# Optimization experiments

Measured on AMD Instinct MI355X. Metric: run time of the kernel, lower is better.

## Reference

```python
import jax, jax.numpy as jnp
import numpy as np

TOP_K = 2


def setup_inputs() -> dict:
    key = jax.random.key(0)
    ks = jax.random.split(key, 5)
    B, S, H, E, F = 4, 1024, 1024, 16, 4096
    scale = 0.02
    return {
        "input_tensor": jax.random.normal(ks[0], (B, S, H), dtype=jnp.float32),
        "Wg": scale * jax.random.normal(ks[1], (H, E), dtype=jnp.float32),
        "bg": jnp.zeros((E,), dtype=jnp.float32),
        "W1": scale * jax.random.normal(ks[2], (E, H, F), dtype=jnp.float32),
        "b1": jnp.zeros((E, F), dtype=jnp.float32),
        "W2": scale * jax.random.normal(ks[3], (E, F, H), dtype=jnp.float32),
        "b2": jnp.zeros((E, H), dtype=jnp.float32),
    }


def reference(input_tensor, Wg, bg, W1, b1, W2, b2):
    # Faithful to DualOutputMoE.forward_first_pass: the per-(b,s,k) Python loop
    # plus _weighted_sum collapses ALL token expert outputs into a single
    # [1,1,H] vector normalized by the total routing weight (= B*S).
    B, S, H = input_tensor.shape
    T = B * S
    E = Wg.shape[1]
    x = input_tensor.reshape(T, H)

    routing_scores = x @ Wg + bg                    # [T, E] (raw gate logits)
    top_v, top_i = jax.lax.top_k(routing_scores, TOP_K)
    top_w = jax.nn.softmax(top_v, axis=-1)          # per-token top-k weights

    # combine[t, e] = sum_k top_w[t, k] * 1[top_i[t, k] == e]
    combine = jnp.zeros((T, E), x.dtype).at[jnp.arange(T)[:, None], top_i].add(top_w)
    total_weight = top_w.sum()                      # matches python sum of .item()s

    def expert_step(acc, params):
        w1, bb1, w2, bb2, c = params                # c: [T] combine weights for this expert
        y = jax.nn.gelu(x @ w1 + bb1, approximate=False) @ w2 + bb2  # [T, H]
        return acc + c @ y, None

    acc0 = jnp.zeros((H,), x.dtype)
    acc, _ = jax.lax.scan(expert_step, acc0, (W1, b1, W2, b2, combine.T))
    first_output = (acc / total_weight).reshape(1, 1, H)
    return first_output
```

## Files before the change

kernel.cpp:

```cpp
#include <hip/hip_runtime.h>
#include <hip/hip_bf16.h>
#include <math.h>

typedef __bf16 bf16_t;
typedef __bf16 bf16x4 __attribute__((ext_vector_type(4)));
typedef __bf16 bf16x8 __attribute__((ext_vector_type(8)));
typedef float  f32x4  __attribute__((ext_vector_type(4)));

#define T_TOK 4096
#define H_DIM 1024
#define E_NUM 16
#define F_DIM 4096
#define CH_ROWS 128
#define CH_MAX  32

#define WS_E0     0
#define WS_E1     16384
#define WS_W0     32768
#define WS_W1     49152
#define WS_COUNTS 65536
#define WS_SUMW   65664
#define WS_XOFF   65792
#define WS_LIDX   131072
#define WS_LW     393216
#define WS_GPART  655360
#define WS_P2     655360
#define WS_G      9043968
#define WS_XE     9306112
#define WS_W1T    30277632
#define W1T_PER_E 8388608

#define AS_GLOBAL(p) ((const __attribute__((address_space(1))) void*)(p))
#define AS_LDS(p)    ((__attribute__((address_space(3))) void*)(p))

__global__ __launch_bounds__(64) void k_route(const float* __restrict__ x,
    const float* __restrict__ Wg, const float* __restrict__ bg,
    int* __restrict__ e0, int* __restrict__ e1,
    float* __restrict__ w0, float* __restrict__ w1)
{
    const int t = blockIdx.x;
    const int lane = threadIdx.x;
    const float* xr = x + (size_t)t * H_DIM;

    float s[E_NUM];
#pragma unroll
    for (int e = 0; e < E_NUM; ++e) s[e] = 0.f;

#pragma unroll
    for (int i = 0; i < 16; ++i) {
        const int h = i * 64 + lane;
        const float xv = xr[h];
        const float4* wr = (const float4*)(Wg + (size_t)h * E_NUM);
        float4 q0 = wr[0], q1 = wr[1], q2 = wr[2], q3 = wr[3];
        s[0] += xv*q0.x;  s[1] += xv*q0.y;  s[2] += xv*q0.z;  s[3] += xv*q0.w;
        s[4] += xv*q1.x;  s[5] += xv*q1.y;  s[6] += xv*q1.z;  s[7] += xv*q1.w;
        s[8] += xv*q2.x;  s[9] += xv*q2.y;  s[10]+= xv*q2.z;  s[11]+= xv*q2.w;
        s[12]+= xv*q3.x;  s[13]+= xv*q3.y;  s[14]+= xv*q3.z;  s[15]+= xv*q3.w;
    }
#pragma unroll
    for (int off = 32; off >= 1; off >>= 1) {
#pragma unroll
        for (int e = 0; e < E_NUM; ++e) s[e] += __shfl_xor(s[e], off);
    }
    if (lane == 0) {
#pragma unroll
        for (int e = 0; e < E_NUM; ++e) s[e] += bg[e];
        float b1v = -3e38f; int i1 = 0;
#pragma unroll
        for (int e = 0; e < E_NUM; ++e) { if (s[e] > b1v) { b1v = s[e]; i1 = e; } }
        float b2v = -3e38f; int i2 = 0;
#pragma unroll
        for (int e = 0; e < E_NUM; ++e) { if (e != i1 && s[e] > b2v) { b2v = s[e]; i2 = e; } }
        const float ex  = expf(b2v - b1v);
        const float inv = 1.f / (1.f + ex);
        e0[t] = i1; e1[t] = i2;
        w0[t] = inv; w1[t] = ex * inv;
    }
}

__global__ __launch_bounds__(64) void k_lists(const int* __restrict__ e0, const int* __restrict__ e1,
    const float* __restrict__ w0, const float* __restrict__ w1,
    int* __restrict__ lidx, float* __restrict__ lw,
    int* __restrict__ counts, float* __restrict__ sumw)
{
    const int e = blockIdx.x;
    const int lane = threadIdx.x;
    int cnt = 0; float sw = 0.f;
    for (int base = 0; base < T_TOK; base += 64) {
        const int t = base + lane;
        const bool m0 = (e0[t] == e);
        const bool m1 = (e1[t] == e);
        const bool m  = m0 | m1;
        const unsigned long long bal = __ballot(m);
        const int pos = cnt + __popcll(bal & ((1ull << lane) - 1ull));
        if (m) {
            const float w = m0 ? w0[t] : w1[t];
            lidx[e * T_TOK + pos] = t;
            lw[e * T_TOK + pos]   = w;
            sw += w;
        }
        cnt += __popcll(bal);
    }
#pragma unroll
    for (int off = 32; off >= 1; off >>= 1) sw += __shfl_xor(sw, off);
    if (lane == 0) { counts[e] = cnt; sumw[e] = sw; }
}

__global__ void k_scan(const int* __restrict__ counts, int* __restrict__ xoff) {
    if (threadIdx.x == 0) {
        int o = 0;
        for (int e = 0; e < E_NUM; ++e) { xoff[e] = o; o += (counts[e] + CH_ROWS - 1) & ~(CH_ROWS - 1); }
    }
}

__global__ __launch_bounds__(256) void k_gather(const float* __restrict__ x,
    const int* __restrict__ lidx, const int* __restrict__ counts,
    const int* __restrict__ xoff, bf16_t* __restrict__ Xe)
{
    const int chunk = blockIdx.x >> 1;
    const int part  = blockIdx.x & 1;
    const int e = blockIdx.y;
    const int cnt = counts[e];
    const int start = chunk * CH_ROWS;
    if (chunk && start >= cnt) return;
    const int tid = threadIdx.x;
    const size_t base = ((size_t)(xoff[e] >> 7) + chunk) * 131072;

    for (int it = 0; it < 32; ++it) {
        const int u    = part * 8192 + it * 256 + tid;
        const int kt   = u >> 10;
        const int wi   = u & 1023;
        const int rl   = wi >> 3;
        const int c    = wi & 7;
        const int row  = start + rl;
        bf16x8 v8 = {};
        if (row < cnt) {
            const int tok = lidx[e * T_TOK + row];
            const int cp  = c ^ (rl & 7);
            const int k   = kt * 64 + cp * 8;
            const float4 a = *(const float4*)(x + (size_t)tok * H_DIM + k);
            const float4 b = *(const float4*)(x + (size_t)tok * H_DIM + k + 4);
            v8[0]=(bf16_t)a.x; v8[1]=(bf16_t)a.y; v8[2]=(bf16_t)a.z; v8[3]=(bf16_t)a.w;
            v8[4]=(bf16_t)b.x; v8[5]=(bf16_t)b.y; v8[6]=(bf16_t)b.z; v8[7]=(bf16_t)b.w;
        }
        *(bf16x8*)(Xe + base + (size_t)kt * 8192 + rl * 64 + c * 8) = v8;
    }
}

__global__ __launch_bounds__(512, 1) void k_w1t(const float* __restrict__ W1,
    bf16_t* __restrict__ W1T, int ebase)
{
    const int kt = blockIdx.x;
    const int fq = blockIdx.y;
    const int ge = blockIdx.z;
    const int e  = ebase + ge;
    const int tid = threadIdx.x;

    __shared__ bf16_t S[64][1024];

    const float* src = W1 + (size_t)e * H_DIM * F_DIM + (size_t)(kt * 64) * F_DIM + fq * 1024;
    for (int it = 0; it < 32; ++it) {
        const int u   = it * 512 + tid;
        const int row = u >> 8;
        const int c4  = u & 255;
        const float4 v = *(const float4*)(src + (size_t)row * F_DIM + c4 * 4);
        bf16x4 b4; b4[0]=(bf16_t)v.x; b4[1]=(bf16_t)v.y; b4[2]=(bf16_t)v.z; b4[3]=(bf16_t)v.w;
        *(bf16x4*)&S[row][c4 * 4] = b4;
    }
    __syncthreads();

#pragma unroll
    for (int ot = 0; ot < 2; ++ot) {
        const int orow = ot * 512 + tid;
        const int ftl  = orow >> 7;
        const int f    = orow & 127;
        const int fg   = ftl * 128 + f;
        bf16_t kv[64];
#pragma unroll
        for (int k = 0; k < 64; ++k) kv[k] = S[k][fg];
        bf16_t* dst = W1T + ((((size_t)ge * 32 + (fq * 8 + ftl)) * 16 + kt) * 8192) + f * 64;
#pragma unroll
        for (int j = 0; j < 8; ++j) {
            bf16x8 pk;
#pragma unroll
            for (int q = 0; q < 8; ++q) pk[q] = kv[j * 8 + q];
            *(bf16x8*)&dst[((j ^ (f & 7)) * 8)] = pk;
        }
    }
}

__global__ __launch_bounds__(256, 2) void k_expert(
    const bf16_t* __restrict__ W1T, const float* __restrict__ b1,
    const bf16_t* __restrict__ Xe, const float* __restrict__ lw,
    const int* __restrict__ counts, const int* __restrict__ xoff,
    float* __restrict__ gpart, int ebase)
{
    const int ftile = blockIdx.x;
    const int chunk = blockIdx.y;
    const int ge    = blockIdx.z;
    const int e     = ebase + ge;
    const int cnt   = counts[e];
    const int start = chunk * CH_ROWS;
    if (chunk && start >= cnt) return;

    __shared__ __align__(16) bf16_t Alds[2][8192];
    __shared__ __align__(16) bf16_t Blds[2][8192];
    __shared__ float w_s[CH_ROWS];
    __shared__ float b1_s[128];
    __shared__ float gred[2][128];

    const int tid  = threadIdx.x;
    const int lane = tid & 63;
    const int wid  = tid >> 6;
    const int wm   = wid & 1;
    const int wn   = wid >> 1;
    const int lr   = lane & 15;
    const int lg   = lane >> 4;

    if (tid < CH_ROWS) {
        const int r = start + tid;
        w_s[tid] = (r < cnt) ? lw[e * T_TOK + r] : 0.f;
    }
    if (tid < 128) b1_s[tid] = b1[(size_t)e * F_DIM + ftile * 128 + tid];

    f32x4 acc[4][4];
#pragma unroll
    for (int i = 0; i < 4; ++i)
#pragma unroll
        for (int j = 0; j < 4; ++j)
#pragma unroll
            for (int q = 0; q < 4; ++q) acc[i][j][q] = 0.f;

    const bf16_t* XeSlab = Xe + ((size_t)(xoff[e] >> 7) + chunk) * 131072;
    const bf16_t* W1Slab = W1T + (((size_t)ge * 32 + ftile) * 16) * 8192;

#define STAGE(T, BUF) { \
    const bf16_t* sa = XeSlab + (size_t)(T) * 8192; \
    const bf16_t* sb = W1Slab + (size_t)(T) * 8192; \
    _Pragma("unroll") \
    for (int p = 0; p < 4; ++p) { \
        const int off = p * 2048 + wid * 512; \
        __builtin_amdgcn_global_load_lds(AS_GLOBAL(sa + off + lane * 8), AS_LDS(&Alds[BUF][off]), 16, 0, 0); \
        __builtin_amdgcn_global_load_lds(AS_GLOBAL(sb + off + lane * 8), AS_LDS(&Blds[BUF][off]), 16, 0, 0); \
    } }

#define COMPUTE(BUF) { \
    _Pragma("unroll") \
    for (int kh = 0; kh < 2; ++kh) { \
        bf16x8 af[4], bfr[4]; \
        _Pragma("unroll") \
        for (int mf = 0; mf < 4; ++mf) { \
            const int r = wm * 64 + mf * 16 + lr; \
            af[mf] = *(const bf16x8*)&Alds[BUF][r * 64 + (((kh << 2) | lg) ^ (r & 7)) * 8]; \
        } \
        _Pragma("unroll") \
        for (int nf = 0; nf < 4; ++nf) { \
            const int f = wn * 64 + nf * 16 + lr; \
            bfr[nf] = *(const bf16x8*)&Blds[BUF][f * 64 + (((kh << 2) | lg) ^ (f & 7)) * 8]; \
        } \
        _Pragma("unroll") \
        for (int mf = 0; mf < 4; ++mf) \
            _Pragma("unroll") \
            for (int nf = 0; nf < 4; ++nf) \
                acc[mf][nf] = __builtin_amdgcn_mfma_f32_16x16x32_bf16(af[mf], bfr[nf], acc[mf][nf], 0, 0, 0); \
    } }

    STAGE(0, 0);
    __syncthreads();

    int cur = 0;
#pragma unroll 2
    for (int t = 0; t < 16; ++t) {
        if (t < 15) { STAGE(t + 1, cur ^ 1); }
        __builtin_amdgcn_sched_barrier(0);
        COMPUTE(cur);
        __syncthreads();
        cur ^= 1;
    }
#undef STAGE
#undef COMPUTE

    float gcol[4] = {0.f, 0.f, 0.f, 0.f};
#pragma unroll
    for (int nf = 0; nf < 4; ++nf) {
        const float bb = b1_s[wn * 64 + nf * 16 + lr];
#pragma unroll
        for (int mf = 0; mf < 4; ++mf) {
#pragma unroll
            for (int i = 0; i < 4; ++i) {
                const int row = wm * 64 + mf * 16 + lg * 4 + i;
                const float h  = acc[mf][nf][i] + bb;
                const float gl = 0.5f * h * (1.f + erff(h * 0.70710678118654752f));
                gcol[nf] += w_s[row] * gl;
            }
        }
    }
#pragma unroll
    for (int nf = 0; nf < 4; ++nf) {
        gcol[nf] += __shfl_xor(gcol[nf], 16);
        gcol[nf] += __shfl_xor(gcol[nf], 32);
    }
    if (lane < 16) {
#pragma unroll
        for (int nf = 0; nf < 4; ++nf) gred[wm][wn * 64 + nf * 16 + lane] = gcol[nf];
    }
    __syncthreads();
    if (tid < 128) {
        const float sum = gred[0][tid] + gred[1][tid];
        gpart[(size_t)(e * CH_MAX + chunk) * F_DIM + ftile * 128 + tid] = sum;
    }
}

__global__ __launch_bounds__(256) void k_redg(const float* __restrict__ gpart,
    const int* __restrict__ counts, float* __restrict__ g)
{
    const int e = blockIdx.y;
    const int f = blockIdx.x * 256 + threadIdx.x;
    const int nch = (counts[e] + CH_ROWS - 1) / CH_ROWS;
    float s = 0.f;
    for (int c = 0; c < nch; ++c)
        s += gpart[(size_t)(e * CH_MAX + c) * F_DIM + f];
    g[(size_t)e * F_DIM + f] = s;
}

__global__ __launch_bounds__(256) void k_out1(const float* __restrict__ g,
    const float* __restrict__ W2, float* __restrict__ p2)
{
    const int fc = blockIdx.x;
    const int e  = blockIdx.y;
    const int tid = threadIdx.x;
    __shared__ float gs[128];
    if (tid < 128) gs[tid] = g[(size_t)e * F_DIM + fc * 128 + tid];
    __syncthreads();
    const float* W2p = W2 + (size_t)e * F_DIM * H_DIM + (size_t)fc * 128 * H_DIM;
    float ax = 0.f, ay = 0.f, az = 0.f, aw = 0.f;
#pragma unroll 8
    for (int f = 0; f < 128; ++f) {
        const float gv = gs[f];
        const float4 wv = *(const float4*)(W2p + (size_t)f * H_DIM + tid * 4);
        ax += gv * wv.x; ay += gv * wv.y; az += gv * wv.z; aw += gv * wv.w;
    }
    float4 st; st.x = ax; st.y = ay; st.z = az; st.w = aw;
    *(float4*)(p2 + (size_t)(e * 32 + fc) * H_DIM + tid * 4) = st;
}

__global__ __launch_bounds__(256) void k_out2(const float* __restrict__ p2,
    const float* __restrict__ sumw, const float* __restrict__ b2, float* __restrict__ out)
{
    const int tid = threadIdx.x;
    const int hh  = tid & 31;
    const int seg = tid >> 5;
    const int h   = blockIdx.x * 32 + hh;
    float s = 0.f;
    for (int j = 0; j < 64; ++j)
        s += p2[(size_t)(seg * 64 + j) * H_DIM + h];
    __shared__ float red[8][33];
    red[seg][hh] = s;
    __syncthreads();
    if (tid < 32) {
        const int h2 = blockIdx.x * 32 + tid;
        float tot = 0.f;
#pragma unroll
        for (int q = 0; q < 8; ++q) tot += red[q][tid];
        float tw = 0.f, bias = 0.f;
#pragma unroll
        for (int e = 0; e < E_NUM; ++e) { tw += sumw[e]; bias += sumw[e] * b2[e * H_DIM + h2]; }
        out[h2] = (tot + bias) / tw;
    }
}

extern "C" void kernel_launch(void* const* d_in, const int* in_sizes, int n_in,
                              void* d_out, int out_size, void* d_ws, size_t ws_size,
                              hipStream_t stream) {
    const float* x  = (const float*)d_in[0];
    const float* Wg = (const float*)d_in[1];
    const float* bg = (const float*)d_in[2];
    const float* W1 = (const float*)d_in[3];
    const float* b1 = (const float*)d_in[4];
    const float* W2 = (const float*)d_in[5];
    const float* b2 = (const float*)d_in[6];
    float* out = (float*)d_out;

    char* ws = (char*)d_ws;
    int*    e0     = (int*)(ws + WS_E0);
    int*    e1     = (int*)(ws + WS_E1);
    float*  w0     = (float*)(ws + WS_W0);
    float*  w1     = (float*)(ws + WS_W1);
    int*    counts = (int*)(ws + WS_COUNTS);
    float*  sumw   = (float*)(ws + WS_SUMW);
    int*    xoff   = (int*)(ws + WS_XOFF);
    int*    lidx   = (int*)(ws + WS_LIDX);
    float*  lw     = (float*)(ws + WS_LW);
    float*  gpart  = (float*)(ws + WS_GPART);
    float*  g      = (float*)(ws + WS_G);
    float*  p2     = (float*)(ws + WS_P2);
    bf16_t* Xe     = (bf16_t*)(ws + WS_XE);
    bf16_t* W1T    = (bf16_t*)(ws + WS_W1T);

    int cap = 1;
    if (ws_size > (size_t)WS_W1T + (size_t)W1T_PER_E) {
        size_t c = (ws_size - (size_t)WS_W1T) / (size_t)W1T_PER_E;
        cap = (c >= 16) ? 16 : (int)c;
        if (cap < 1) cap = 1;
    }

    k_route<<<T_TOK, 64, 0, stream>>>(x, Wg, bg, e0, e1, w0, w1);
    k_lists<<<E_NUM, 64, 0, stream>>>(e0, e1, w0, w1, lidx, lw, counts, sumw);
    k_scan<<<1, 64, 0, stream>>>(counts, xoff);
    k_gather<<<dim3(CH_MAX * 2, E_NUM), 256, 0, stream>>>(x, lidx, counts, xoff, Xe);
    for (int eb = 0; eb < E_NUM; eb += cap) {
        const int gN = (E_NUM - eb < cap) ? (E_NUM - eb) : cap;
        k_w1t<<<dim3(16, 4, gN), 512, 0, stream>>>(W1, W1T, eb);
        k_expert<<<dim3(32, CH_MAX, gN), 256, 0, stream>>>(W1T, b1, Xe, lw, counts, xoff, gpart, eb);
    }
    k_redg<<<dim3(F_DIM / 256, E_NUM), 256, 0, stream>>>(gpart, counts, g);
    k_out1<<<dim3(32, E_NUM), 256, 0, stream>>>(g, W2, p2);
    k_out2<<<32, 256, 0, stream>>>(p2, sumw, b2, out);
}
```

Measured before the change: 367.6 us.

## Fuse W1 fp32-to-bf16 transpose into expert GEMM B-tile loading

Removes the separate k_w1t pass that converted and transposed W1 into a bf16 workspace. The expert GEMM now reads fp32 W1 straight into registers, converts it to bf16 and writes it swizzled into LDS, overlapping that work with compute through register prefetch. This drops a full write and reread of the bf16 W1 copy and lets all experts launch in one grid. The cost is that each chunk block re-reads fp32 W1 (twice the bytes, with up to 32 chunks per ftile), and the strided scalar loads and extra registers may lower occupancy. k_route also packs four tokens per 256-thread block.

Measured after the change: 314.3 us. 1.17x faster.

```diff
diff --git a/kernel.cpp b/kernel.cpp
--- a/kernel.cpp
+++ b/kernel.cpp
@@ -27,19 +27,17 @@
 #define WS_P2     655360
 #define WS_G      9043968
 #define WS_XE     9306112
-#define WS_W1T    30277632
-#define W1T_PER_E 8388608
 
 #define AS_GLOBAL(p) ((const __attribute__((address_space(1))) void*)(p))
 #define AS_LDS(p)    ((__attribute__((address_space(3))) void*)(p))
 
-__global__ __launch_bounds__(64) void k_route(const float* __restrict__ x,
+__global__ __launch_bounds__(256) void k_route(const float* __restrict__ x,
     const float* __restrict__ Wg, const float* __restrict__ bg,
     int* __restrict__ e0, int* __restrict__ e1,
     float* __restrict__ w0, float* __restrict__ w1)
 {
-    const int t = blockIdx.x;
-    const int lane = threadIdx.x;
+    const int t = blockIdx.x * 4 + (threadIdx.x >> 6);
+    const int lane = threadIdx.x & 63;
     const float* xr = x + (size_t)t * H_DIM;
 
     float s[E_NUM];
@@ -147,58 +145,15 @@
     }
 }
 
-__global__ __launch_bounds__(512, 1) void k_w1t(const float* __restrict__ W1,
-    bf16_t* __restrict__ W1T, int ebase)
-{
-    const int kt = blockIdx.x;
-    const int fq = blockIdx.y;
-    const int ge = blockIdx.z;
-    const int e  = ebase + ge;
-    const int tid = threadIdx.x;
-
-    __shared__ bf16_t S[64][1024];
-
-    const float* src = W1 + (size_t)e * H_DIM * F_DIM + (size_t)(kt * 64) * F_DIM + fq * 1024;
-    for (int it = 0; it < 32; ++it) {
-        const int u   = it * 512 + tid;
-        const int row = u >> 8;
-        const int c4  = u & 255;
-        const float4 v = *(const float4*)(src + (size_t)row * F_DIM + c4 * 4);
-        bf16x4 b4; b4[0]=(bf16_t)v.x; b4[1]=(bf16_t)v.y; b4[2]=(bf16_t)v.z; b4[3]=(bf16_t)v.w;
-        *(bf16x4*)&S[row][c4 * 4] = b4;
-    }
-    __syncthreads();
-
-#pragma unroll
-    for (int ot = 0; ot < 2; ++ot) {
-        const int orow = ot * 512 + tid;
-        const int ftl  = orow >> 7;
-        const int f    = orow & 127;
-        const int fg   = ftl * 128 + f;
-        bf16_t kv[64];
-#pragma unroll
-        for (int k = 0; k < 64; ++k) kv[k] = S[k][fg];
-        bf16_t* dst = W1T + ((((size_t)ge * 32 + (fq * 8 + ftl)) * 16 + kt) * 8192) + f * 64;
-#pragma unroll
-        for (int j = 0; j < 8; ++j) {
-            bf16x8 pk;
-#pragma unroll
-            for (int q = 0; q < 8; ++q) pk[q] = kv[j * 8 + q];
-            *(bf16x8*)&dst[((j ^ (f & 7)) * 8)] = pk;
-        }
-    }
-}
-
 __global__ __launch_bounds__(256, 2) void k_expert(
-    const bf16_t* __restrict__ W1T, const float* __restrict__ b1,
+    const float* __restrict__ W1, const float* __restrict__ b1,
     const bf16_t* __restrict__ Xe, const float* __restrict__ lw,
     const int* __restrict__ counts, const int* __restrict__ xoff,
-    float* __restrict__ gpart, int ebase)
+    float* __restrict__ gpart)
 {
     const int ftile = blockIdx.x;
     const int chunk = blockIdx.y;
-    const int ge    = blockIdx.z;
-    const int e     = ebase + ge;
+    const int e     = blockIdx.z;
     const int cnt   = counts[e];
     const int start = chunk * CH_ROWS;
     if (chunk && start >= cnt) return;
@@ -232,16 +187,36 @@
             for (int q = 0; q < 4; ++q) acc[i][j][q] = 0.f;
 
     const bf16_t* XeSlab = Xe + ((size_t)(xoff[e] >> 7) + chunk) * 131072;
-    const bf16_t* W1Slab = W1T + (((size_t)ge * 32 + ftile) * 16) * 8192;
-
-#define STAGE(T, BUF) { \
-    const bf16_t* sa = XeSlab + (size_t)(T) * 8192; \
-    const bf16_t* sb = W1Slab + (size_t)(T) * 8192; \
+
+    const int bf_ = tid & 127;
+    const int kh2 = tid >> 7;
+    const int fsw = bf_ & 7;
+    const float* W1p = W1 + (size_t)e * H_DIM * F_DIM + (size_t)(kh2 * 32) * F_DIM
+                       + (size_t)ftile * 128 + bf_;
+
+    float bv[32];
+
+#define ISSUE_A(T, BUF) { \
     _Pragma("unroll") \
     for (int p = 0; p < 4; ++p) { \
         const int off = p * 2048 + wid * 512; \
-        __builtin_amdgcn_global_load_lds(AS_GLOBAL(sa + off + lane * 8), AS_LDS(&Alds[BUF][off]), 16, 0, 0); \
-        __builtin_amdgcn_global_load_lds(AS_GLOBAL(sb + off + lane * 8), AS_LDS(&Blds[BUF][off]), 16, 0, 0); \
+        __builtin_amdgcn_global_load_lds(AS_GLOBAL(XeSlab + (size_t)(T) * 8192 + off + lane * 8), \
+            AS_LDS(&Alds[BUF][off]), 16, 0, 0); \
+    } }
+
+#define ISSUE_B(T) { \
+    const float* wp = W1p + (size_t)(T) * 64 * F_DIM; \
+    _Pragma("unroll") \
+    for (int j = 0; j < 32; ++j) bv[j] = wp[(size_t)j * F_DIM]; }
+
+#define WRITE_B(BUF) { \
+    _Pragma("unroll") \
+    for (int c = 0; c < 4; ++c) { \
+        bf16x8 pk; \
+        _Pragma("unroll") \
+        for (int q = 0; q < 8; ++q) pk[q] = (bf16_t)bv[c * 8 + q]; \
+        const int kslot = kh2 * 4 + c; \
+        *(bf16x8*)&Blds[BUF][bf_ * 64 + (kslot ^ fsw) * 8] = pk; \
     } }
 
 #define COMPUTE(BUF) { \
@@ -265,19 +240,26 @@
                 acc[mf][nf] = __builtin_amdgcn_mfma_f32_16x16x32_bf16(af[mf], bfr[nf], acc[mf][nf], 0, 0, 0); \
     } }
 
-    STAGE(0, 0);
+    ISSUE_B(0);
+    ISSUE_A(0, 0);
+    WRITE_B(0);
     __syncthreads();
 
     int cur = 0;
-#pragma unroll 2
     for (int t = 0; t < 16; ++t) {
-        if (t < 15) { STAGE(t + 1, cur ^ 1); }
+        if (t < 15) {
+            ISSUE_B(t + 1);
+            ISSUE_A(t + 1, cur ^ 1);
+        }
         __builtin_amdgcn_sched_barrier(0);
         COMPUTE(cur);
+        if (t < 15) WRITE_B(cur ^ 1);
         __syncthreads();
         cur ^= 1;
     }
-#undef STAGE
+#undef ISSUE_A
+#undef ISSUE_B
+#undef WRITE_B
 #undef COMPUTE
 
     float gcol[4] = {0.f, 0.f, 0.f, 0.f};
@@ -395,24 +377,12 @@
     float*  g      = (float*)(ws + WS_G);
     float*  p2     = (float*)(ws + WS_P2);
     bf16_t* Xe     = (bf16_t*)(ws + WS_XE);
-    bf16_t* W1T    = (bf16_t*)(ws + WS_W1T);
-
-    int cap = 1;
-    if (ws_size > (size_t)WS_W1T + (size_t)W1T_PER_E) {
-        size_t c = (ws_size - (size_t)WS_W1T) / (size_t)W1T_PER_E;
-        cap = (c >= 16) ? 16 : (int)c;
-        if (cap < 1) cap = 1;
-    }
-
-    k_route<<<T_TOK, 64, 0, stream>>>(x, Wg, bg, e0, e1, w0, w1);
+
+    k_route<<<T_TOK / 4, 256, 0, stream>>>(x, Wg, bg, e0, e1, w0, w1);
     k_lists<<<E_NUM, 64, 0, stream>>>(e0, e1, w0, w1, lidx, lw, counts, sumw);
     k_scan<<<1, 64, 0, stream>>>(counts, xoff);
     k_gather<<<dim3(CH_MAX * 2, E_NUM), 256, 0, stream>>>(x, lidx, counts, xoff, Xe);
-    for (int eb = 0; eb < E_NUM; eb += cap) {
-        const int gN = (E_NUM - eb < cap) ? (E_NUM - eb) : cap;
-        k_w1t<<<dim3(16, 4, gN), 512, 0, stream>>>(W1, W1T, eb);
-        k_expert<<<dim3(32, CH_MAX, gN), 256, 0, stream>>>(W1T, b1, Xe, lw, counts, xoff, gpart, eb);
-    }
+    k_expert<<<dim3(32, CH_MAX, E_NUM), 256, 0, stream>>>(W1, b1, Xe, lw, counts, xoff, gpart);
     k_redg<<<dim3(F_DIM / 256, E_NUM), 256, 0, stream>>>(gpart, counts, g);
     k_out1<<<dim3(32, E_NUM), 256, 0, stream>>>(g, W2, p2);
     k_out2<<<32, 256, 0, stream>>>(p2, sumw, b2, out);
```
